# Performance work log

Measured on AMD Instinct MI355X. Metric: run time of the kernel, lower is better.

Reference implementation:

```python
import jax, jax.numpy as jnp
import numpy as np

EPS = 1e-12  # F.normalize default eps


def setup_inputs() -> dict:
    key = jax.random.key(0)
    k1, k2, k3, k4 = jax.random.split(key, 4)
    B, N, C, NH = 8, 4096, 512, 8
    x = jax.random.normal(k1, (B, N, C), dtype=jnp.float32)
    Wqkv = jax.random.normal(k2, (3 * C, C), dtype=jnp.float32) * 0.02
    Wproj = jax.random.normal(k3, (C, C), dtype=jnp.float32) * 0.02
    bproj = jax.random.normal(k4, (C,), dtype=jnp.float32) * 0.01
    temp = jnp.ones((NH, 1, 1), dtype=jnp.float32)
    return {"x": x, "Wqkv": Wqkv, "Wproj": Wproj, "bproj": bproj,
            "temp": temp, "H": 64, "W": 64}


def _l2norm(t):
    # normalize along last axis, matching F.normalize(p=2, eps=1e-12)
    return t / jnp.maximum(jnp.linalg.norm(t, axis=-1, keepdims=True), EPS)


def reference(x, Wqkv, Wproj, bproj, temp, H, W):
    B, N, C = x.shape
    nh = temp.shape[0]
    hd = C // nh
    # qkv projection: [B, N, 3, nh, hd]
    qkv = jnp.einsum('bnc,dc->bnd', x, Wqkv).reshape(B, N, 3, nh, hd)
    q = qkv[:, :, 0]  # [B, N, nh, hd]
    k = qkv[:, :, 1]
    v = qkv[:, :, 2]
    # transpose to [B, nh, hd, N] and L2-normalize along tokens (N)
    qn = _l2norm(q.transpose(0, 2, 3, 1))
    kn = _l2norm(k.transpose(0, 2, 3, 1))
    vt = v.transpose(0, 2, 3, 1)  # [B, nh, hd, N]
    # channel attention: [B, nh, hd, hd], scaled by learned per-head temp
    attn = jax.nn.softmax(jnp.einsum('bhcn,bhdn->bhcd', qn, kn) * temp, axis=-1)
    # [B, nh, hd, N] -> [B, N, nh, hd] -> [B, N, C]
    out = jnp.einsum('bhcd,bhdn->bhcn', attn, vt).transpose(0, 3, 1, 2).reshape(B, N, C)
    return jnp.einsum('bnc,dc->bnd', out, Wproj) + bproj
```

## Files before the change

### kernel.cpp

```cpp
#include <hip/hip_runtime.h>
#include <stdint.h>

#define DEVI __device__ __forceinline__

typedef __attribute__((ext_vector_type(8))) short bf16x8;
typedef __attribute__((ext_vector_type(4))) float f32x4;
typedef __attribute__((ext_vector_type(4))) unsigned short u16x4;
typedef __attribute__((ext_vector_type(4))) float float4v;

DEVI unsigned short f2bf(float f) {
  unsigned int u = __builtin_bit_cast(unsigned int, f);
  u += 0x7FFFu + ((u >> 16) & 1u);
  return (unsigned short)(u >> 16);
}
DEVI float bf2f(short s) {
  unsigned int u = ((unsigned int)(unsigned short)s) << 16;
  return __builtin_bit_cast(float, u);
}
DEVI void gload16(const unsigned short* g, unsigned short* l) {
  __builtin_amdgcn_global_load_lds(
      (const __attribute__((address_space(1))) unsigned int*)g,
      (__attribute__((address_space(3))) unsigned int*)l, 16, 0, 0);
}

__global__ void cast_prep(const float* __restrict__ x,
                          unsigned short* __restrict__ Xbf,
                          unsigned short* __restrict__ xT,
                          const float* __restrict__ Wqkv,
                          unsigned short* __restrict__ Wqk,
                          unsigned short* __restrict__ WvT) {
  __shared__ float tls[64 * 129];
  const int t = threadIdx.x;
  if (blockIdx.z < 8) {
    const int n0 = blockIdx.x * 128, c0 = blockIdx.y * 64, b = blockIdx.z;
    const int q = t & 15;
    const int nl = t >> 4;
#pragma unroll
    for (int i = 0; i < 8; ++i) {
      const int n = i * 16 + nl;
      const size_t gi = ((size_t)b * 4096 + n0 + n) * 512 + c0 + q * 4;
      float4v f = *(const float4v*)&x[gi];
      u16x4 o;
      o.x = f2bf(f.x); o.y = f2bf(f.y); o.z = f2bf(f.z); o.w = f2bf(f.w);
      *(u16x4*)&Xbf[gi] = o;
      tls[(q * 4 + 0) * 129 + n] = f.x;
      tls[(q * 4 + 1) * 129 + n] = f.y;
      tls[(q * 4 + 2) * 129 + n] = f.z;
      tls[(q * 4 + 3) * 129 + n] = f.w;
    }
    __syncthreads();
    const int cr = t >> 2, nq = t & 3;
#pragma unroll
    for (int ii = 0; ii < 4; ++ii) {
      const int n = nq * 8 + ii * 32;
      bf16x8 o;
#pragma unroll
      for (int s = 0; s < 8; ++s) o[s] = (short)f2bf(tls[cr * 129 + n + s]);
      *(bf16x8*)&xT[((size_t)b * 512 + c0 + cr) * 4096 + n0 + n] = o;
    }
    return;
  }
  const int id = blockIdx.y * 32 + blockIdx.x;
  {
    const float4v* src = (const float4v*)Wqkv;
    u16x4* dst = (u16x4*)Wqk;
    int base = id * 512 + t;
#pragma unroll
    for (int j = 0; j < 2; ++j) {
      int i = base + j * 256;
      float4v f = src[i];
      u16x4 o;
      o.x = f2bf(f.x); o.y = f2bf(f.y); o.z = f2bf(f.z); o.w = f2bf(f.w);
      dst[i] = o;
    }
  }
  if (id < 64) {
    const int tr = id >> 3, tc = id & 7;
    const int c = t & 63, rb = t >> 6;
    __syncthreads();
#pragma unroll
    for (int rr = 0; rr < 16; ++rr) {
      int r = rb * 16 + rr;
      tls[r * 65 + c] = Wqkv[(size_t)(1024 + tr * 64 + r) * 512 + tc * 64 + c];
    }
    __syncthreads();
#pragma unroll
    for (int rr = 0; rr < 16; ++rr) {
      int j = rb * 16 + rr;
      WvT[(size_t)(tc * 64 + j) * 512 + tr * 64 + c] = f2bf(tls[c * 65 + j]);
    }
  }
}

#define STAGE256(kt)                                                         \
  {                                                                          \
    const int bo_ = ((kt) & 1) * 16384;                                      \
    _Pragma("unroll") for (int i_ = 0; i_ < 4; ++i_) {                       \
      gload16(pA + (size_t)i_ * 64 * strideA + (kt) * 64,                    \
              ldsA + bo_ + i_ * 4096 + wave * 512);                          \
      gload16(pB + (size_t)i_ * 64 * strideB + (kt) * 64,                    \
              ldsB + bo_ + i_ * 4096 + wave * 512);                          \
    }                                                                        \
  }

template <int NT>
DEVI void gemm256_loop(const unsigned short* pA, size_t strideA,
                       const unsigned short* pB, size_t strideB,
                       unsigned short* ldsA, unsigned short* ldsB,
                       int wave, int lane, f32x4 acc[8][4]) {
  const int wr = wave >> 2, wc = wave & 3;
  const int fr = lane & 15, kg = lane >> 4;
  const int x0 = ((kg * 16) ^ ((fr & 7) << 4)) >> 1;
  const int x1 = ((64 + kg * 16) ^ ((fr & 7) << 4)) >> 1;
  STAGE256(0);
  for (int kt = 0; kt < NT; ++kt) {
    __builtin_amdgcn_s_barrier();
    __builtin_amdgcn_sched_barrier(0);
    if (kt + 1 < NT) {
      STAGE256(kt + 1);
      asm volatile("s_waitcnt vmcnt(8)" ::: "memory");
    } else {
      asm volatile("s_waitcnt vmcnt(0)" ::: "memory");
    }
    __builtin_amdgcn_sched_barrier(0);
    __builtin_amdgcn_s_barrier();
    __builtin_amdgcn_sched_barrier(0);
    const int bo = (kt & 1) * 16384;
    bf16x8 bfrag[4][2];
#pragma unroll
    for (int n = 0; n < 4; ++n) {
      const int ro = (wc * 64 + n * 16 + fr) * 64;
      bfrag[n][0] = *(const bf16x8*)&ldsB[bo + ro + x0];
      bfrag[n][1] = *(const bf16x8*)&ldsB[bo + ro + x1];
    }
#pragma unroll
    for (int mp = 0; mp < 4; ++mp) {
      bf16x8 af[2][2];
#pragma unroll
      for (int mi = 0; mi < 2; ++mi) {
        const int ro = (wr * 128 + (mp * 2 + mi) * 16 + fr) * 64;
        af[mi][0] = *(const bf16x8*)&ldsA[bo + ro + x0];
        af[mi][1] = *(const bf16x8*)&ldsA[bo + ro + x1];
      }
      __builtin_amdgcn_s_setprio(1);
#pragma unroll
      for (int mi = 0; mi < 2; ++mi)
#pragma unroll
        for (int n = 0; n < 4; ++n) {
          acc[mp * 2 + mi][n] = __builtin_amdgcn_mfma_f32_16x16x32_bf16(
              af[mi][0], bfrag[n][0], acc[mp * 2 + mi][n], 0, 0, 0);
          acc[mp * 2 + mi][n] = __builtin_amdgcn_mfma_f32_16x16x32_bf16(
              af[mi][1], bfrag[n][1], acc[mp * 2 + mi][n], 0, 0, 0);
        }
      __builtin_amdgcn_s_setprio(0);
    }
  }
}

__launch_bounds__(512, 2)
__global__ void gsyrk(const unsigned short* __restrict__ xT,
                      unsigned short* __restrict__ Gpart) {
  __shared__ __align__(16) unsigned short ldsA[2 * 16384];
  __shared__ __align__(16) unsigned short ldsB[2 * 16384];
  const int tid = threadIdx.x, wave = tid >> 6, lane = tid & 63;
  const int tc = blockIdx.x >> 1, td = blockIdx.x & 1;
  const int chunk = blockIdx.y, b = blockIdx.z;
  const unsigned short* xb = xT + (size_t)b * 512 * 4096 + chunk * 512;
  const int sRow = tid >> 3;
  const int kEl = 8 * ((tid & 7) ^ ((tid >> 3) & 7));
  const unsigned short* pA = xb + (size_t)(tc * 256 + sRow) * 4096 + kEl;
  const unsigned short* pB = xb + (size_t)(td * 256 + sRow) * 4096 + kEl;
  f32x4 acc[8][4] = {};
  gemm256_loop<8>(pA, 4096, pB, 4096, ldsA, ldsB, wave, lane, acc);
  const int wr = wave >> 2, wc = wave & 3;
  const int fr = lane & 15, kg = lane >> 4;
  unsigned short* Gp = Gpart + (size_t)(chunk * 8 + b) * 512 * 512;
#pragma unroll
  for (int m = 0; m < 8; ++m) {
    const int row0 = tc * 256 + wr * 128 + m * 16 + kg * 4;
#pragma unroll
    for (int n = 0; n < 4; ++n) {
      const int col = td * 256 + wc * 64 + n * 16 + fr;
      f32x4 v = acc[m][n];
#pragma unroll
      for (int r = 0; r < 4; ++r)
        Gp[(size_t)(row0 + r) * 512 + col] = f2bf(v[r]);
    }
  }
}

__global__ void greduce(const unsigned short* __restrict__ Gpart,
                        unsigned short* __restrict__ Gbf) {
  const int stride = gridDim.x * blockDim.x;
  const int n4 = 8 * 512 * 512 / 4;
  for (int i = blockIdx.x * blockDim.x + threadIdx.x; i < n4; i += stride) {
    const int b = i >> 16, j4 = i & 65535;
    float s0 = 0, s1 = 0, s2 = 0, s3 = 0;
#pragma unroll
    for (int c = 0; c < 8; ++c) {
      u16x4 v = ((const u16x4*)Gpart)[(size_t)(c * 8 + b) * 65536 + j4];
      s0 += bf2f((short)v.x); s1 += bf2f((short)v.y);
      s2 += bf2f((short)v.z); s3 += bf2f((short)v.w);
    }
    u16x4 o;
    o.x = f2bf(s0); o.y = f2bf(s1); o.z = f2bf(s2); o.w = f2bf(s3);
    ((u16x4*)Gbf)[i] = o;
  }
}

template <int KITERS>
DEVI void gemm_db(const unsigned short* gA, int strideA,
                  const unsigned short* gB, int strideB,
                  unsigned short (*lA)[4096], unsigned short (*lB)[4096],
                  int wave, int wr, int wc, int fr, int kg, f32x4 acc[4][4]) {
  const int wo = wave * 512;
#define STAGE_T(buf, kk)                                                    \
  gload16(gA + (kk) * 32, lA[buf] + wo);                                    \
  gload16(gA + (kk) * 32 + (size_t)64 * strideA, lA[buf] + wo + 2048);      \
  gload16(gB + (kk) * 32, lB[buf] + wo);                                    \
  gload16(gB + (kk) * 32 + (size_t)64 * strideB, lB[buf] + wo + 2048);
  STAGE_T(0, 0);
  __syncthreads();
  int cur = 0;
  for (int kk = 1; kk <= KITERS; ++kk) {
    if (kk < KITERS) { STAGE_T(cur ^ 1, kk); }
    bf16x8 af[4], bfv[4];
#pragma unroll
    for (int mi = 0; mi < 4; ++mi)
      af[mi] = *(const bf16x8*)&lA[cur][(wr * 64 + mi * 16 + fr) * 32 + kg * 8];
#pragma unroll
    for (int ni = 0; ni < 4; ++ni)
      bfv[ni] = *(const bf16x8*)&lB[cur][(wc * 64 + ni * 16 + fr) * 32 + kg * 8];
#pragma unroll
    for (int mi = 0; mi < 4; ++mi)
#pragma unroll
      for (int ni = 0; ni < 4; ++ni)
        acc[mi][ni] = __builtin_amdgcn_mfma_f32_16x16x32_bf16(
            af[mi], bfv[ni], acc[mi][ni], 0, 0, 0);
    __syncthreads();
    cur ^= 1;
  }
#undef STAGE_T
}

__launch_bounds__(256)
__global__ void tall_gemm(const unsigned short* __restrict__ Wqk,
                          const unsigned short* __restrict__ Gbf,
                          unsigned short* __restrict__ Tbf,
                          float* __restrict__ ssPart) {
  __shared__ __align__(16) unsigned short lA[2][4096];
  __shared__ __align__(16) unsigned short lB[2][4096];
  __shared__ float ssL[128][2];
  const int tid = threadIdx.x, wave = tid >> 6, lane = tid & 63;
  const int wr = wave >> 1, wc = wave & 1, fr = lane & 15, kg = lane >> 4;
  const int rowBase = blockIdx.x * 128, colBase = blockIdx.y * 128;
  const int b = blockIdx.z;
  const unsigned short* Gb = Gbf + (size_t)b * 512 * 512;
  f32x4 acc[4][4] = {};
  const int sRow = wave * 16 + (lane >> 2);
  const int sK = (lane & 3) * 8;
  gemm_db<16>(Wqk + (size_t)(rowBase + sRow) * 512 + sK, 512,
              Gb + (size_t)(colBase + sRow) * 512 + sK, 512,
              lA, lB, wave, wr, wc, fr, kg, acc);
  unsigned short* Tb = Tbf + (size_t)b * 1024 * 512;
#pragma unroll
  for (int mi = 0; mi < 4; ++mi) {
    const int rbase = rowBase + wr * 64 + mi * 16 + kg * 4;
    f32x4 sacc = {0.f, 0.f, 0.f, 0.f};
#pragma unroll
    for (int ni = 0; ni < 4; ++ni) {
      const int col = colBase + wc * 64 + ni * 16 + fr;
      f32x4 v = acc[mi][ni];
#pragma unroll
      for (int r = 0; r < 4; ++r) {
        float w = bf2f((short)Wqk[(size_t)(rbase + r) * 512 + col]);
        Tb[(size_t)(rbase + r) * 512 + col] = f2bf(v[r]);
        sacc[r] += v[r] * w;
      }
    }
#pragma unroll
    for (int o = 1; o < 16; o <<= 1) {
#pragma unroll
      for (int r = 0; r < 4; ++r) sacc[r] += __shfl_xor(sacc[r], o);
    }
    if (fr == 0) {
#pragma unroll
      for (int r = 0; r < 4; ++r)
        ssL[wr * 64 + mi * 16 + kg * 4 + r][wc] = sacc[r];
    }
  }
  __syncthreads();
  if (tid < 128)
    ssPart[((size_t)blockIdx.y * 8 + b) * 1024 + rowBase + tid] =
        ssL[tid][0] + ssL[tid][1];
}

__global__ void s_softmax(const unsigned short* __restrict__ Tbf,
                          const unsigned short* __restrict__ Wqk,
                          const float* __restrict__ ssPart,
                          const float* __restrict__ temp,
                          float* __restrict__ attnOut) {
  __shared__ float Sl[64 * 64];
  __shared__ float invq[64], invk[64];
  const int bh = blockIdx.x, b = bh >> 3, h = bh & 7;
  const unsigned short* qbase = Tbf + (size_t)(b * 1024 + h * 64) * 512;
  const unsigned short* kbase = Wqk + (size_t)(512 + h * 64) * 512;
  const int t = threadIdx.x;
  const int wave = t >> 6, lane = t & 63;
  const int wr = wave >> 1, wc = wave & 1, fr = lane & 15, kg = lane >> 4;
  f32x4 acc[2][2] = {};
  for (int kk = 0; kk < 512; kk += 32) {
    bf16x8 a[2], bb[2];
#pragma unroll
    for (int mi = 0; mi < 2; ++mi)
      a[mi] = *(const bf16x8*)(qbase + (size_t)(wr * 32 + mi * 16 + fr) * 512 + kk + kg * 8);
#pragma unroll
    for (int ni = 0; ni < 2; ++ni)
      bb[ni] = *(const bf16x8*)(kbase + (size_t)(wc * 32 + ni * 16 + fr) * 512 + kk + kg * 8);
#pragma unroll
    for (int mi = 0; mi < 2; ++mi)
#pragma unroll
      for (int ni = 0; ni < 2; ++ni)
        acc[mi][ni] = __builtin_amdgcn_mfma_f32_16x16x32_bf16(a[mi], bb[ni], acc[mi][ni], 0, 0, 0);
  }
#pragma unroll
  for (int mi = 0; mi < 2; ++mi)
#pragma unroll
    for (int ni = 0; ni < 2; ++ni) {
      f32x4 v = acc[mi][ni];
#pragma unroll
      for (int r = 0; r < 4; ++r)
        Sl[(wr * 32 + mi * 16 + kg * 4 + r) * 64 + wc * 32 + ni * 16 + fr] = v[r];
    }
  if (t < 128) {
    const int r = (t >> 6) * 512 + h * 64 + (t & 63);
    float s = 0.f;
#pragma unroll
    for (int nt = 0; nt < 4; ++nt) s += ssPart[((size_t)nt * 8 + b) * 1024 + r];
    float inv = 1.f / fmaxf(sqrtf(s), 1e-12f);
    if (t < 64) invq[t] = inv;
    else invk[t - 64] = inv;
  }
  __syncthreads();
  const float tmp = temp[h];
  const int c = t >> 2, q4 = t & 3;
  float lg[16];
  float mx = -1e30f;
#pragma unroll
  for (int j = 0; j < 16; ++j) {
    const int d = q4 * 16 + j;
    lg[j] = Sl[c * 64 + d] * invq[c] * invk[d] * tmp;
    mx = fmaxf(mx, lg[j]);
  }
  mx = fmaxf(mx, __shfl_xor(mx, 1));
  mx = fmaxf(mx, __shfl_xor(mx, 2));
  float sum = 0.f;
#pragma unroll
  for (int j = 0; j < 16; ++j) {
    lg[j] = __expf(lg[j] - mx);
    sum += lg[j];
  }
  sum += __shfl_xor(sum, 1);
  sum += __shfl_xor(sum, 2);
  const float inv = 1.f / sum;
#pragma unroll
  for (int j = 0; j < 16; ++j)
    attnOut[(size_t)bh * 4096 + c * 64 + q4 * 16 + j] = lg[j] * inv;
}

__global__ void weff_kernel(const float* __restrict__ attn,
                            const float* __restrict__ Wproj,
                            unsigned short* __restrict__ Weff) {
  const int bh = blockIdx.x, eb = blockIdx.y;
  const int b = bh >> 3, h = bh & 7;
  __shared__ float at[64 * 64];
  for (int i = threadIdx.x; i < 4096; i += 256)
    at[i] = attn[(size_t)bh * 4096 + i];
  __syncthreads();
  const int e = eb * 64 + (threadIdx.x >> 2);
  const int dq = threadIdx.x & 3;
  float acc[16] = {};
  const float* wrow = Wproj + (size_t)e * 512 + h * 64;
  for (int c = 0; c < 64; ++c) {
    const float w = wrow[c];
#pragma unroll
    for (int j = 0; j < 16; ++j) acc[j] += w * at[c * 64 + dq * 16 + j];
  }
  unsigned short* outp = Weff + ((size_t)b * 512 + e) * 512 + h * 64 + dq * 16;
#pragma unroll
  for (int j = 0; j < 16; ++j) outp[j] = f2bf(acc[j]);
}

__launch_bounds__(256)
__global__ void wcomb_gemm(const unsigned short* __restrict__ WeffAll,
                           const unsigned short* __restrict__ WvT,
                           unsigned short* __restrict__ WcombAll) {
  __shared__ __align__(16) unsigned short lA[2][4096];
  __shared__ __align__(16) unsigned short lB[2][4096];
  const int tid = threadIdx.x, wave = tid >> 6, lane = tid & 63;
  const int wr = wave >> 1, wc = wave & 1, fr = lane & 15, kg = lane >> 4;
  const int b = blockIdx.z;
  const int rowBase = blockIdx.x * 128, colBase = blockIdx.y * 128;
  const unsigned short* A = WeffAll + (size_t)b * 512 * 512;
  f32x4 acc[4][4] = {};
  const int sRow = wave * 16 + (lane >> 2);
  const int sK = (lane & 3) * 8;
  gemm_db<16>(A + (size_t)(rowBase + sRow) * 512 + sK, 512,
              WvT + (size_t)(colBase + sRow) * 512 + sK, 512,
              lA, lB, wave, wr, wc, fr, kg, acc);
  unsigned short* Wc = WcombAll + (size_t)b * 512 * 512;
#pragma unroll
  for (int mi = 0; mi < 4; ++mi) {
    const int rbase = rowBase + wr * 64 + mi * 16 + kg * 4;
#pragma unroll
    for (int ni = 0; ni < 4; ++ni) {
      const int col = colBase + wc * 64 + ni * 16 + fr;
      f32x4 v = acc[mi][ni];
#pragma unroll
      for (int r = 0; r < 4; ++r)
        Wc[(size_t)(rbase + r) * 512 + col] = f2bf(v[r]);
    }
  }
}

__launch_bounds__(512, 2)
__global__ void out_gemm(const unsigned short* __restrict__ Xbf,
                         const unsigned short* __restrict__ WcombAll,
                         const float* __restrict__ bias,
                         float* __restrict__ out) {
  __shared__ __align__(16) unsigned short ldsA[2 * 16384];
  __shared__ __align__(16) unsigned short ldsB[2 * 16384];
  const int tid = threadIdx.x, wave = tid >> 6, lane = tid & 63;
  const int b = blockIdx.z;
  const int rowBase = blockIdx.x * 256, colBase = blockIdx.y * 256;
  const unsigned short* A = Xbf + (size_t)b * 4096 * 512;
  const unsigned short* Bw = WcombAll + (size_t)b * 512 * 512;
  const int sRow = tid >> 3;
  const int kEl = 8 * ((tid & 7) ^ ((tid >> 3) & 7));
  const unsigned short* pA = A + (size_t)(rowBase + sRow) * 512 + kEl;
  const unsigned short* pB = Bw + (size_t)(colBase + sRow) * 512 + kEl;
  f32x4 acc[8][4] = {};
  gemm256_loop<8>(pA, 512, pB, 512, ldsA, ldsB, wave, lane, acc);
  const int wr = wave >> 2, wc = wave & 3;
  const int fr = lane & 15, kg = lane >> 4;
#pragma unroll
  for (int m = 0; m < 8; ++m) {
    const int row0 = rowBase + wr * 128 + m * 16 + kg * 4;
#pragma unroll
    for (int n = 0; n < 4; ++n) {
      const int col = colBase + wc * 64 + n * 16 + fr;
      const float bcol = bias[col];
      f32x4 v = acc[m][n];
#pragma unroll
      for (int r = 0; r < 4; ++r)
        out[((size_t)b * 4096 + row0 + r) * 512 + col] = v[r] + bcol;
    }
  }
}

extern "C" void kernel_launch(void* const* d_in, const int* in_sizes, int n_in,
                              void* d_out, int out_size, void* d_ws, size_t ws_size,
                              hipStream_t stream) {
  const float* x = (const float*)d_in[0];
  const float* Wqkv = (const float*)d_in[1];
  const float* Wproj = (const float*)d_in[2];
  const float* bproj = (const float*)d_in[3];
  const float* temp = (const float*)d_in[4];
  float* out = (float*)d_out;

  char* ws = (char*)d_ws;
  unsigned short* Xbf = (unsigned short*)(ws + 0);
  unsigned short* xT = (unsigned short*)(ws + 33554432);
  unsigned short* Wqk = (unsigned short*)(ws + 67108864);
  unsigned short* WvT = (unsigned short*)(ws + 68157440);
  unsigned short* Gpart = (unsigned short*)(ws + 68681728);
  unsigned short* Gbf = (unsigned short*)(ws + 102236160);
  unsigned short* Tbf = (unsigned short*)(ws + 106430464);
  float* ssPart = (float*)(ws + 114819072);
  float* attn = (float*)(ws + 114950144);
  unsigned short* Weff = (unsigned short*)(ws + 115998720);
  unsigned short* Wcomb = (unsigned short*)(ws + 120193024);

  cast_prep<<<dim3(32, 8, 9), 256, 0, stream>>>(x, Xbf, xT, Wqkv, Wqk, WvT);
  gsyrk<<<dim3(4, 8, 8), 512, 0, stream>>>(xT, Gpart);
  greduce<<<1024, 256, 0, stream>>>(Gpart, Gbf);
  tall_gemm<<<dim3(8, 4, 8), 256, 0, stream>>>(Wqk, Gbf, Tbf, ssPart);
  s_softmax<<<64, 256, 0, stream>>>(Tbf, Wqk, ssPart, temp, attn);
  weff_kernel<<<dim3(64, 8), 256, 0, stream>>>(attn, Wproj, Weff);
  wcomb_gemm<<<dim3(4, 4, 8), 256, 0, stream>>>(Weff, WvT, Wcomb);
  out_gemm<<<dim3(16, 2, 8), 512, 0, stream>>>(Xbf, Wcomb, bproj, out);
}
```

Baseline: 130.4 us.

## Fuse Weff computation into softmax via MFMA, remap block order, skip unused T stores

```diff
diff --git a/kernel.cpp b/kernel.cpp
--- a/kernel.cpp
+++ b/kernel.cpp
@@ -28,7 +28,9 @@
                           unsigned short* __restrict__ xT,
                           const float* __restrict__ Wqkv,
                           unsigned short* __restrict__ Wqk,
-                          unsigned short* __restrict__ WvT) {
+                          unsigned short* __restrict__ WvT,
+                          const float* __restrict__ Wproj,
+                          unsigned short* __restrict__ WpBf) {
   __shared__ float tls[64 * 129];
   const int t = threadIdx.x;
   if (blockIdx.z < 8) {
@@ -58,6 +60,15 @@
       for (int s = 0; s < 8; ++s) o[s] = (short)f2bf(tls[cr * 129 + n + s]);
       *(bf16x8*)&xT[((size_t)b * 512 + c0 + cr) * 4096 + n0 + n] = o;
     }
+    return;
+  }
+  if (blockIdx.z == 9) {
+    const int id = blockIdx.y * 32 + blockIdx.x;
+    const int i = id * 256 + t;
+    float4v f = ((const float4v*)Wproj)[i];
+    u16x4 o;
+    o.x = f2bf(f.x); o.y = f2bf(f.y); o.z = f2bf(f.z); o.w = f2bf(f.w);
+    ((u16x4*)WpBf)[i] = o;
     return;
   }
   const int id = blockIdx.y * 32 + blockIdx.x;
@@ -162,9 +173,11 @@
                       unsigned short* __restrict__ Gpart) {
   __shared__ __align__(16) unsigned short ldsA[2 * 16384];
   __shared__ __align__(16) unsigned short ldsB[2 * 16384];
+  int fl = blockIdx.x + 4 * (blockIdx.y + 8 * blockIdx.z);
+  fl = (fl & 7) * 32 + (fl >> 3);
+  const int quad = fl & 3, chunk = (fl >> 2) & 7, b = fl >> 5;
   const int tid = threadIdx.x, wave = tid >> 6, lane = tid & 63;
-  const int tc = blockIdx.x >> 1, td = blockIdx.x & 1;
-  const int chunk = blockIdx.y, b = blockIdx.z;
+  const int tc = quad >> 1, td = quad & 1;
   const unsigned short* xb = xT + (size_t)b * 512 * 4096 + chunk * 512;
   const int sRow = tid >> 3;
   const int kEl = 8 * ((tid & 7) ^ ((tid >> 3) & 7));
@@ -263,6 +276,7 @@
               Gb + (size_t)(colBase + sRow) * 512 + sK, 512,
               lA, lB, wave, wr, wc, fr, kg, acc);
   unsigned short* Tb = Tbf + (size_t)b * 1024 * 512;
+  const bool wT = rowBase < 512;
 #pragma unroll
   for (int mi = 0; mi < 4; ++mi) {
     const int rbase = rowBase + wr * 64 + mi * 16 + kg * 4;
@@ -274,7 +288,7 @@
 #pragma unroll
       for (int r = 0; r < 4; ++r) {
         float w = bf2f((short)Wqk[(size_t)(rbase + r) * 512 + col]);
-        Tb[(size_t)(rbase + r) * 512 + col] = f2bf(v[r]);
+        if (wT) Tb[(size_t)(rbase + r) * 512 + col] = f2bf(v[r]);
         sacc[r] += v[r] * w;
       }
     }
@@ -299,9 +313,11 @@
                           const unsigned short* __restrict__ Wqk,
                           const float* __restrict__ ssPart,
                           const float* __restrict__ temp,
-                          float* __restrict__ attnOut) {
+                          const unsigned short* __restrict__ WpBf,
+                          unsigned short* __restrict__ Weff) {
   __shared__ float Sl[64 * 64];
   __shared__ float invq[64], invk[64];
+  __shared__ __align__(16) unsigned short atT[64 * 72];
   const int bh = blockIdx.x, b = bh >> 3, h = bh & 7;
   const unsigned short* qbase = Tbf + (size_t)(b * 1024 + h * 64) * 512;
   const unsigned short* kbase = Wqk + (size_t)(512 + h * 64) * 512;
@@ -365,30 +381,37 @@
   const float inv = 1.f / sum;
 #pragma unroll
   for (int j = 0; j < 16; ++j)
-    attnOut[(size_t)bh * 4096 + c * 64 + q4 * 16 + j] = lg[j] * inv;
-}
-
-__global__ void weff_kernel(const float* __restrict__ attn,
-                            const float* __restrict__ Wproj,
-                            unsigned short* __restrict__ Weff) {
-  const int bh = blockIdx.x, eb = blockIdx.y;
-  const int b = bh >> 3, h = bh & 7;
-  __shared__ float at[64 * 64];
-  for (int i = threadIdx.x; i < 4096; i += 256)
-    at[i] = attn[(size_t)bh * 4096 + i];
+    atT[(q4 * 16 + j) * 72 + c] = f2bf(lg[j] * inv);
   __syncthreads();
-  const int e = eb * 64 + (threadIdx.x >> 2);
-  const int dq = threadIdx.x & 3;
-  float acc[16] = {};
-  const float* wrow = Wproj + (size_t)e * 512 + h * 64;
-  for (int c = 0; c < 64; ++c) {
-    const float w = wrow[c];
-#pragma unroll
-    for (int j = 0; j < 16; ++j) acc[j] += w * at[c * 64 + dq * 16 + j];
-  }
-  unsigned short* outp = Weff + ((size_t)b * 512 + e) * 512 + h * 64 + dq * 16;
-#pragma unroll
-  for (int j = 0; j < 16; ++j) outp[j] = f2bf(acc[j]);
+  bf16x8 bfrag[4][2];
+#pragma unroll
+  for (int n = 0; n < 4; ++n)
+#pragma unroll
+    for (int kk = 0; kk < 2; ++kk)
+      bfrag[n][kk] =
+          *(const bf16x8*)&atT[(n * 16 + fr) * 72 + kk * 32 + kg * 8];
+  unsigned short* We = Weff + (size_t)b * 512 * 512 + h * 64;
+#pragma unroll
+  for (int m = 0; m < 8; ++m) {
+    const int eA = wave * 128 + m * 16 + fr;
+    bf16x8 af[2];
+#pragma unroll
+    for (int kk = 0; kk < 2; ++kk)
+      af[kk] = *(const bf16x8*)&WpBf[(size_t)eA * 512 + h * 64 + kk * 32 + kg * 8];
+    f32x4 acc4[4] = {};
+#pragma unroll
+    for (int kk = 0; kk < 2; ++kk)
+#pragma unroll
+      for (int n = 0; n < 4; ++n)
+        acc4[n] = __builtin_amdgcn_mfma_f32_16x16x32_bf16(af[kk], bfrag[n][kk],
+                                                          acc4[n], 0, 0, 0);
+    const int e0 = wave * 128 + m * 16 + kg * 4;
+#pragma unroll
+    for (int n = 0; n < 4; ++n)
+#pragma unroll
+      for (int r = 0; r < 4; ++r)
+        We[(size_t)(e0 + r) * 512 + n * 16 + fr] = f2bf(acc4[n][r]);
+  }
 }
 
 __launch_bounds__(256)
@@ -430,9 +453,11 @@
                          float* __restrict__ out) {
   __shared__ __align__(16) unsigned short ldsA[2 * 16384];
   __shared__ __align__(16) unsigned short ldsB[2 * 16384];
+  int fl = blockIdx.x + 16 * (blockIdx.y + 2 * blockIdx.z);
+  fl = (fl & 7) * 32 + (fl >> 3);
+  const int bxi = fl & 15, byi = (fl >> 4) & 1, b = fl >> 5;
   const int tid = threadIdx.x, wave = tid >> 6, lane = tid & 63;
-  const int b = blockIdx.z;
-  const int rowBase = blockIdx.x * 256, colBase = blockIdx.y * 256;
+  const int rowBase = bxi * 256, colBase = byi * 256;
   const unsigned short* A = Xbf + (size_t)b * 4096 * 512;
   const unsigned short* Bw = WcombAll + (size_t)b * 512 * 512;
   const int sRow = tid >> 3;
@@ -477,16 +502,16 @@
   unsigned short* Gbf = (unsigned short*)(ws + 102236160);
   unsigned short* Tbf = (unsigned short*)(ws + 106430464);
   float* ssPart = (float*)(ws + 114819072);
-  float* attn = (float*)(ws + 114950144);
   unsigned short* Weff = (unsigned short*)(ws + 115998720);
   unsigned short* Wcomb = (unsigned short*)(ws + 120193024);
-
-  cast_prep<<<dim3(32, 8, 9), 256, 0, stream>>>(x, Xbf, xT, Wqkv, Wqk, WvT);
+  unsigned short* WpBf = (unsigned short*)(ws + 124387328);
+
+  cast_prep<<<dim3(32, 8, 10), 256, 0, stream>>>(x, Xbf, xT, Wqkv, Wqk, WvT,
+                                                 Wproj, WpBf);
   gsyrk<<<dim3(4, 8, 8), 512, 0, stream>>>(xT, Gpart);
   greduce<<<1024, 256, 0, stream>>>(Gpart, Gbf);
   tall_gemm<<<dim3(8, 4, 8), 256, 0, stream>>>(Wqk, Gbf, Tbf, ssPart);
-  s_softmax<<<64, 256, 0, stream>>>(Tbf, Wqk, ssPart, temp, attn);
-  weff_kernel<<<dim3(64, 8), 256, 0, stream>>>(attn, Wproj, Weff);
+  s_softmax<<<64, 256, 0, stream>>>(Tbf, Wqk, ssPart, temp, WpBf, Weff);
   wcomb_gemm<<<dim3(4, 4, 8), 256, 0, stream>>>(Weff, WvT, Wcomb);
   out_gemm<<<dim3(16, 2, 8), 512, 0, stream>>>(Xbf, Wcomb, bproj, out);
 }
```

Result: faster. 127.2 us (-2.5%).
